# Kernel tuning notes

Hardware: AMD Instinct MI355X
Metric: run time of the kernel (lower is better)

## Reference

```python
import jax, jax.numpy as jnp
import numpy as np
from jax import lax

H_IMG = 224
NUM_HEADS = 8
EPS = 1e-5


def setup_inputs() -> dict:
    key = jax.random.key(0)
    ks = jax.random.split(key, 16)
    C, Dff = 256, 512
    conv_s = 1.0 / np.sqrt(C * 9)
    lin_s = 1.0 / np.sqrt(C)
    lin2_s = 1.0 / np.sqrt(Dff)
    inp = {
        'lidar': jax.random.normal(ks[0], (2, C, H_IMG, H_IMG), jnp.float32),
        'image': jax.random.normal(ks[1], (2, C, H_IMG, H_IMG), jnp.float32),
        'cl_w': jax.random.normal(ks[2], (C, C, 3, 3), jnp.float32) * conv_s,
        'cl_b': jnp.zeros((C,), jnp.float32),
        'bnl_g': jnp.ones((C,), jnp.float32), 'bnl_b': jnp.zeros((C,), jnp.float32),
        'bnl_m': jnp.zeros((C,), jnp.float32), 'bnl_v': jnp.ones((C,), jnp.float32),
        'ci_w': jax.random.normal(ks[3], (C, C, 3, 3), jnp.float32) * conv_s,
        'ci_b': jnp.zeros((C,), jnp.float32),
        'bni_g': jnp.ones((C,), jnp.float32), 'bni_b': jnp.zeros((C,), jnp.float32),
        'bni_m': jnp.zeros((C,), jnp.float32), 'bni_v': jnp.ones((C,), jnp.float32),
        'qw': jax.random.normal(ks[4], (C, C), jnp.float32) * lin_s,
        'qb': jnp.zeros((C,), jnp.float32),
        'kw': jax.random.normal(ks[5], (C, C), jnp.float32) * lin_s,
        'kb': jnp.zeros((C,), jnp.float32),
        'vw': jax.random.normal(ks[6], (C, C), jnp.float32) * lin_s,
        'vb': jnp.zeros((C,), jnp.float32),
        'ow': jax.random.normal(ks[7], (C, C), jnp.float32) * lin_s,
        'ob': jnp.zeros((C,), jnp.float32),
        'ln1_g': jnp.ones((C,), jnp.float32), 'ln1_b': jnp.zeros((C,), jnp.float32),
        'w1': jax.random.normal(ks[8], (C, Dff), jnp.float32) * lin_s,
        'b1': jnp.zeros((Dff,), jnp.float32),
        'w2': jax.random.normal(ks[9], (Dff, C), jnp.float32) * lin2_s,
        'b2': jnp.zeros((C,), jnp.float32),
        'ln2_g': jnp.ones((C,), jnp.float32), 'ln2_b': jnp.zeros((C,), jnp.float32),
        'op_w': jax.random.normal(ks[10], (C, C, 1, 1), jnp.float32) * lin_s,
        'op_b': jnp.zeros((C,), jnp.float32),
        'sp_w': jax.random.normal(ks[11], (C, C, 1, 1), jnp.float32) * lin_s,
        'sp_b': jnp.zeros((C,), jnp.float32),
    }
    return inp


def _conv(x, w, b, stride, pad):
    y = lax.conv_general_dilated(x, w, (stride, stride), ((pad, pad), (pad, pad)),
                                 dimension_numbers=('NCHW', 'OIHW', 'NCHW'))
    return y + b[None, :, None, None]


def _bn(x, g, b, m, v):  # eval-mode BatchNorm2d
    inv = g * lax.rsqrt(v + EPS)
    return x * inv[None, :, None, None] + (b - m * inv)[None, :, None, None]


def _ln(x, g, b):
    mu = jnp.mean(x, -1, keepdims=True)
    var = jnp.mean(jnp.square(x - mu), -1, keepdims=True)
    return (x - mu) * lax.rsqrt(var + EPS) * g + b


def reference(lidar, image, cl_w, cl_b, bnl_g, bnl_b, bnl_m, bnl_v,
              ci_w, ci_b, bni_g, bni_b, bni_m, bni_v,
              qw, qb, kw, kb, vw, vb, ow, ob, ln1_g, ln1_b,
              w1, b1, w2, b2, ln2_g, ln2_b, op_w, op_b, sp_w, sp_b):
    B, C, H, W = lidar.shape
    # spatial compression (stride-4 conv + BN + ReLU)
    lc = jax.nn.relu(_bn(_conv(lidar, cl_w, cl_b, 4, 1), bnl_g, bnl_b, bnl_m, bnl_v))
    ic = jax.nn.relu(_bn(_conv(image, ci_w, ci_b, 4, 1), bni_g, bni_b, bni_m, bni_v))
    _, Ch, Hc, Wc = lc.shape
    N = Hc * Wc
    lseq = lc.reshape(B, Ch, N).transpose(0, 2, 1)  # (B,N,C)
    iseq = ic.reshape(B, Ch, N).transpose(0, 2, 1)

    # cross-attention (lidar queries, image keys/values)
    h, d = NUM_HEADS, Ch // NUM_HEADS
    scale = d ** -0.5
    Q = (lseq @ qw + qb).reshape(B, N, h, d).transpose(0, 2, 1, 3)
    K = (iseq @ kw + kb).reshape(B, N, h, d).transpose(0, 2, 1, 3)
    V = (iseq @ vw + vb).reshape(B, N, h, d).transpose(0, 2, 1, 3)
    scores = jnp.einsum('bhqd,bhkd->bhqk', Q, K) * scale
    attn = jax.nn.softmax(scores, axis=-1)
    ctx = jnp.einsum('bhqk,bhkd->bhqd', attn, V)
    attn_out = ctx.transpose(0, 2, 1, 3).reshape(B, N, Ch) @ ow + ob

    x = _ln(lseq + attn_out, ln1_g, ln1_b)
    ffn = jax.nn.relu(x @ w1 + b1) @ w2 + b2
    x = _ln(x + ffn, ln2_g, ln2_b)

    oc = x.transpose(0, 2, 1).reshape(B, Ch, Hc, Wc)
    up = jax.image.resize(oc, (B, Ch, H, W), method='bilinear')  # align_corners=False semantics
    out = _conv(up, op_w, op_b, 1, 0) + _conv(lidar, sp_w, sp_b, 1, 0)
    return out
```

## Files before the change

kernel.cpp:

```cpp
#include <hip/hip_runtime.h>
#include <hip/hip_bf16.h>

typedef __bf16 bf16;
typedef __attribute__((ext_vector_type(8))) __bf16 bf16x8;
typedef __attribute__((ext_vector_type(4))) __bf16 bf16x4;
typedef __attribute__((ext_vector_type(4))) float f32x4;
typedef __attribute__((ext_vector_type(4))) unsigned int u32x4;

#define LN_EPS 1e-5f

__device__ __forceinline__ void gload16(const void* g, void* l) {
  __builtin_amdgcn_global_load_lds(
      (__attribute__((address_space(1))) void*)g,
      (__attribute__((address_space(3))) void*)l, 16, 0, 0);
}

__device__ __forceinline__ unsigned pk2(float a, float b) {
  unsigned ua = __builtin_bit_cast(unsigned short, (bf16)a);
  unsigned ub = __builtin_bit_cast(unsigned short, (bf16)b);
  return ua | (ub << 16);
}

__device__ __forceinline__ float fexp2(float x) {
  float r;
  asm("v_exp_f32 %0, %1" : "=v"(r) : "v"(x));
  return r;
}


__global__ void bn_prep2_k(const float* cb0, const float* g0, const float* b0,
                           const float* m0, const float* v0, float* sc0, float* sh0,
                           const float* cb1, const float* g1, const float* b1,
                           const float* m1, const float* v1, float* sc1, float* sh1,
                           float* zp) {
  int c = threadIdx.x;
  bool z = blockIdx.x != 0;
  const float* cb = z ? cb1 : cb0;
  const float* g = z ? g1 : g0;
  const float* bb = z ? b1 : b0;
  const float* m = z ? m1 : m0;
  const float* v = z ? v1 : v0;
  float* sc = z ? sc1 : sc0;
  float* sh = z ? sh1 : sh0;
  float s = g[c] * rsqrtf(v[c] + LN_EPS);
  sc[c] = s;
  sh[c] = (cb[c] - m[c]) * s + bb[c];
  if (blockIdx.x == 0) zp[c] = 0.f;
}

__global__ void t_cvt4_k(const float* a0, const float* a1, const float* a2,
                         const float* a3, bf16* o0, bf16* o1, bf16* o2, bf16* o3) {
  __shared__ float tile[32][33];
  int z = blockIdx.z;
  const float* in = z == 0 ? a0 : z == 1 ? a1 : z == 2 ? a2 : a3;
  bf16* out = z == 0 ? o0 : z == 1 ? o1 : z == 2 ? o2 : o3;
  int c0 = blockIdx.x * 32, r0 = blockIdx.y * 32;
  int tx = threadIdx.x, ty = threadIdx.y;
  for (int yy = ty; yy < 32; yy += 8)
    tile[yy][tx] = in[(long)(r0 + yy) * 256 + c0 + tx];
  __syncthreads();
  for (int yy = ty; yy < 32; yy += 8)
    out[(long)(c0 + yy) * 256 + r0 + tx] = (bf16)tile[tx][yy];
}

__global__ void t_cvt_k(const float* __restrict__ in, bf16* __restrict__ out,
                        int R, int Cc) {
  __shared__ float tile[32][33];
  int c0 = blockIdx.x * 32, r0 = blockIdx.y * 32;
  int tx = threadIdx.x, ty = threadIdx.y;
  for (int yy = ty; yy < 32; yy += 8)
    tile[yy][tx] = in[(long)(r0 + yy) * Cc + c0 + tx];
  __syncthreads();
  for (int yy = ty; yy < 32; yy += 8)
    out[(long)(c0 + yy) * R + r0 + tx] = (bf16)tile[tx][yy];
}

__global__ void cvt2_k(const float* a0, const float* a1, bf16* o0, bf16* o1, int n) {
  const float* in = blockIdx.y ? a1 : a0;
  bf16* out = blockIdx.y ? o1 : o0;
  int i = (blockIdx.x * 256 + threadIdx.x) * 4;
  if (i < n) {
    float4 v = *(const float4*)(in + i);
    bf16x4 o = {(bf16)v.x, (bf16)v.y, (bf16)v.z, (bf16)v.w};
    *(bf16x4*)(out + i) = o;
  }
}

__global__ void wprep_k(const float* w0, const float* w1, bf16* o0, bf16* o1) {
  const float* w = blockIdx.y ? w1 : w0;
  bf16* o = blockIdx.y ? o1 : o0;
  int idx = blockIdx.x * 256 + threadIdx.x;
  int co = idx / 2304, r = idx - co * 2304;
  int k9 = r >> 8, ci = r & 255;
  o[idx] = (bf16)w[(co * 256 + ci) * 9 + k9];
}

__global__ __launch_bounds__(256) void t_in_k(const float* __restrict__ lid,
                                              const float* __restrict__ img,
                                              bf16* __restrict__ lidT,
                                              bf16* __restrict__ imgT) {
  int z = blockIdx.z;
  int b = z & 1;
  const float* in = (z < 2) ? lid : img;
  bf16* out = (z < 2) ? lidT : imgT;
  long p0 = (long)blockIdx.x * 128;
  int c0 = blockIdx.y * 128;
  __shared__ unsigned tile[128 * 68];
  int t = threadIdx.x;
  const float* ib = in + (long)b * 256 * 50176;
  bf16* ob = out + (long)b * 50176 * 256;
  int q = t & 31;
  int cp = t >> 5;
#pragma unroll
  for (int pp = 0; pp < 8; ++pp) {
    int chl = pp * 16 + cp * 2;
    const float* s = ib + (long)(c0 + chl) * 50176 + p0 + q * 4;
    float4 a = *(const float4*)s;
    float4 bv = *(const float4*)(s + 50176);
    unsigned wv[4] = {pk2(a.x, bv.x), pk2(a.y, bv.y), pk2(a.z, bv.z),
                      pk2(a.w, bv.w)};
    int c = pp * 8 + cp;
#pragma unroll
    for (int j = 0; j < 4; ++j)
      tile[(q * 4 + j) * 68 + c] = wv[j];
  }
  __syncthreads();
  int c8 = t & 15;
#pragma unroll
  for (int pp = 0; pp < 8; ++pp) {
    int p = pp * 16 + (t >> 4);
    u32x4 vv = *(const u32x4*)&tile[p * 68 + c8 * 4];
    *(u32x4*)(ob + (p0 + p) * 256 + c0 + c8 * 8) = vv;
  }
}

__global__ void t_v_k(const bf16* __restrict__ V, bf16* __restrict__ Vt) {
  __shared__ bf16 tile[32][33];
  int b = blockIdx.z;
  int n0 = blockIdx.x * 32, c0 = blockIdx.y * 32;
  int tx = threadIdx.x, ty = threadIdx.y;
  for (int yy = ty; yy < 32; yy += 8)
    tile[yy][tx] = V[(long)(b * 3136 + n0 + yy) * 256 + c0 + tx];
  __syncthreads();
  for (int yy = ty; yy < 32; yy += 8)
    Vt[(long)(b * 256 + c0 + yy) * 3136 + n0 + tx] = tile[tx][yy];
}

__global__ void ln_k(const float* __restrict__ in, const float* __restrict__ g,
                     const float* __restrict__ bb, float* __restrict__ outf,
                     bf16* __restrict__ outb) {
  int w = threadIdx.x >> 6, l = threadIdx.x & 63;
  long row = (long)blockIdx.x * 4 + w;
  float4 v = *(const float4*)(in + row * 256 + l * 4);
  float s = v.x + v.y + v.z + v.w;
  for (int m = 1; m < 64; m <<= 1) s += __shfl_xor(s, m);
  float mu = s * (1.0f / 256.0f);
  float dx = v.x - mu, dy = v.y - mu, dz = v.z - mu, dw = v.w - mu;
  float q = dx * dx + dy * dy + dz * dz + dw * dw;
  for (int m = 1; m < 64; m <<= 1) q += __shfl_xor(q, m);
  float rstd = rsqrtf(q * (1.0f / 256.0f) + LN_EPS);
  int c = l * 4;
  float y0 = dx * rstd * g[c] + bb[c];
  float y1 = dy * rstd * g[c + 1] + bb[c + 1];
  float y2 = dz * rstd * g[c + 2] + bb[c + 2];
  float y3 = dw * rstd * g[c + 3] + bb[c + 3];
  if (outf) {
    float4 o = {y0, y1, y2, y3};
    *(float4*)(outf + row * 256 + c) = o;
  }
  bf16x4 ob = {(bf16)y0, (bf16)y1, (bf16)y2, (bf16)y3};
  *(bf16x4*)(outb + row * 256 + c) = ob;
}

struct ConvJob {
  const bf16* inT;
  const bf16* wT;
  const float* scale;
  const float* shift;
  bf16* out;
};

__global__ __launch_bounds__(256) void convgemm_k(ConvJob j0, ConvJob j1,
                                                  const bf16* zp) {
  const ConvJob jb = blockIdx.z ? j1 : j0;
  __shared__ bf16 lA[64 * 64];
  __shared__ bf16 lB[64 * 64];
  const int tid = threadIdx.x;
  const int w = tid >> 6, l = tid & 63;
  const int l15 = l & 15;
  const int m0 = blockIdx.x * 64;
  const int n0 = blockIdx.y * 64;
  const int mw = (w >> 1) * 32, nw = (w & 1) * 32;
  f32x4 acc[2][2] = {};
  const int srow = w * 8 + (l >> 3);
  const int kc8 = (l & 7) * 8;
  long rb[2];
  int voy[2], vox[2];
#pragma unroll
  for (int p = 0; p < 2; ++p) {
    int m = m0 + srow + p * 32;
    int b = m / 3136;
    int mm = m - b * 3136;
    int oy = mm / 56, ox = mm - oy * 56;
    rb[p] = ((long)b * 50176 + (long)(4 * oy - 1) * 224 + (4 * ox - 1)) * 256 + kc8;
    voy[p] = oy;
    vox[p] = ox;
  }
  const bf16* Bb = jb.wT + (long)(n0 + srow) * 2304 + kc8;
  bf16* lAp = &lA[srow * 64 + kc8];
  bf16* lBp = &lB[srow * 64 + kc8];
  const bf16* zsrc = zp + kc8;
#pragma unroll
  for (int st = 0; st < 36; ++st) {
    const int k9 = st >> 2, ci0 = (st & 3) * 64;
    const int ky = k9 / 3, kx = k9 - 3 * ky;
    const long koff = (long)(ky * 224 + kx) * 256 + ci0;
#pragma unroll
    for (int p = 0; p < 2; ++p) {
      bool ok = (voy[p] > 0 || ky > 0) && (vox[p] > 0 || kx > 0);
      const bf16* src = ok ? jb.inT + rb[p] + koff : zsrc;
      gload16(src, lAp + p * 32 * 64);
    }
    gload16(Bb + st * 64, lBp);
    gload16(Bb + 32 * 2304 + st * 64, lBp + 32 * 64);
    __syncthreads();
    const int kq = (l >> 4) * 8;
#pragma unroll
    for (int kk = 0; kk < 64; kk += 32) {
      bf16x8 af[2], bfv[2];
#pragma unroll
      for (int i = 0; i < 2; ++i)
        af[i] = *(const bf16x8*)&lA[(mw + i * 16 + l15) * 64 + kk + kq];
#pragma unroll
      for (int j = 0; j < 2; ++j)
        bfv[j] = *(const bf16x8*)&lB[(nw + j * 16 + l15) * 64 + kk + kq];
#pragma unroll
      for (int i = 0; i < 2; ++i)
#pragma unroll
        for (int j = 0; j < 2; ++j)
          acc[i][j] = __builtin_amdgcn_mfma_f32_16x16x32_bf16(af[i], bfv[j],
                                                              acc[i][j], 0, 0, 0);
    }
    __syncthreads();
  }
#pragma unroll
  for (int i = 0; i < 2; ++i)
#pragma unroll
    for (int j = 0; j < 2; ++j)
#pragma unroll
      for (int r = 0; r < 4; ++r) {
        const long row = m0 + mw + i * 16 + (l >> 4) * 4 + r;
        const long col = n0 + nw + j * 16 + l15;
        float v = fmaxf(acc[i][j][r] * jb.scale[col] + jb.shift[col], 0.f);
        jb.out[row * 256 + col] = (bf16)v;
      }
}


struct EpiParams {
  float* out0;
  bf16* out1;
  const float* v0;
  const float* res;
  const bf16* resb;
  int ldc;
  float mul;
};

struct GemmJob {
  const bf16* A;
  const bf16* Bt;
  EpiParams ep;
};

struct GemmJobs3 {
  GemmJob j[3];
};

enum { EPI_QKV = 0, EPI_BIAS_RELU_BF16 = 1, EPI_BIAS_ADD = 2,
       EPI_BIAS_ADDB = 3, EPI_ROWB_F32 = 4, EPI_FINAL2 = 5 };

template <int EPI, int BM, int BN>
__global__ __launch_bounds__(256) void gemm_bt(GemmJobs3 jobs, int K) {
  const GemmJob jb = jobs.j[blockIdx.z];
  const bf16* __restrict__ A = jb.A;
  const bf16* __restrict__ Bt = jb.Bt;
  const EpiParams ep = jb.ep;
  constexpr int MI = (BM == 128 && BN == 128) ? 4 : 2;
  constexpr int NJ = (BN == 128) ? 4 : 2;
  __shared__ bf16 lA[BM * 64];
  __shared__ bf16 lB[BN * 64];
  const int tid = threadIdx.x;
  const int w = tid >> 6, l = tid & 63;
  const int l15 = l & 15;
  const long m0 = (long)blockIdx.x * BM;
  const long n0 = (long)blockIdx.y * BN;
  const int mw = (BM == 128) ? ((BN == 128) ? (w >> 1) * 64 : w * 32)
                             : (w >> 1) * 32;
  const int nw = (BN == 128) ? (w & 1) * 64 : ((BM == 128) ? 0 : (w & 1) * 32);
  f32x4 acc[MI][NJ] = {};
  const int srow = w * 8 + (l >> 3);
  const int kc8 = (l & 7) * 8;
  const bf16* Ab = A + (m0 + srow) * (long)K + kc8;
  const bf16* Bb = Bt + (n0 + srow) * (long)K + kc8;
  bf16* lAp = &lA[srow * 64 + kc8];
  bf16* lBp = &lB[srow * 64 + kc8];
  for (int k0 = 0; k0 < K; k0 += 64) {
#pragma unroll
    for (int p = 0; p < BM / 32; ++p)
      gload16(Ab + (long)p * 32 * K + k0, lAp + p * 32 * 64);
#pragma unroll
    for (int p = 0; p < BN / 32; ++p)
      gload16(Bb + (long)p * 32 * K + k0, lBp + p * 32 * 64);
    __syncthreads();
    const int kq = (l >> 4) * 8;
#pragma unroll
    for (int kk = 0; kk < 64; kk += 32) {
      bf16x8 af[MI], bfv[NJ];
#pragma unroll
      for (int i = 0; i < MI; ++i)
        af[i] = *(const bf16x8*)&lA[(mw + i * 16 + l15) * 64 + kk + kq];
#pragma unroll
      for (int j = 0; j < NJ; ++j)
        bfv[j] = *(const bf16x8*)&lB[(nw + j * 16 + l15) * 64 + kk + kq];
#pragma unroll
      for (int i = 0; i < MI; ++i)
#pragma unroll
        for (int j = 0; j < NJ; ++j)
          acc[i][j] = __builtin_amdgcn_mfma_f32_16x16x32_bf16(af[i], bfv[j],
                                                              acc[i][j], 0, 0, 0);
    }
    __syncthreads();
  }
  const int ldc = ep.ldc;
#pragma unroll
  for (int i = 0; i < MI; ++i)
#pragma unroll
    for (int j = 0; j < NJ; ++j)
#pragma unroll
      for (int r = 0; r < 4; ++r) {
        const long row = m0 + mw + i * 16 + (l >> 4) * 4 + r;
        const long col = n0 + nw + j * 16 + l15;
        float v = acc[i][j][r];
        if constexpr (EPI == EPI_QKV) {
          ep.out1[row * ldc + col] = (bf16)((v + ep.v0[col]) * ep.mul);
        } else if constexpr (EPI == EPI_BIAS_RELU_BF16) {
          ep.out1[row * ldc + col] = (bf16)fmaxf(v + ep.v0[col], 0.f);
        } else if constexpr (EPI == EPI_BIAS_ADD) {
          ep.out0[row * ldc + col] = v + ep.v0[col] + ep.res[row * ldc + col];
        } else if constexpr (EPI == EPI_BIAS_ADDB) {
          ep.out0[row * ldc + col] =
              v + ep.v0[col] + (float)ep.resb[row * ldc + col];
        } else if constexpr (EPI == EPI_ROWB_F32) {
          ep.out0[row * ldc + col] = v + ep.v0[row];
        } else {
          int colp = (int)col;
          int y = colp / 224, x = colp - y * 224;
          int ry = y & 3, rx = x & 3;
          int y0 = (y >> 2) - 1 + (ry >> 1);
          int x0 = (x >> 2) - 1 + (rx >> 1);
          float wy = (ry == 0) ? 0.625f : (ry == 1) ? 0.875f : (ry == 2) ? 0.125f : 0.375f;
          float wx = (rx == 0) ? 0.625f : (rx == 1) ? 0.875f : (rx == 2) ? 0.125f : 0.375f;
          int y0c = y0 > 0 ? y0 : 0, y1c = (y0 + 1) < 55 ? (y0 + 1) : 55;
          int x0c = x0 > 0 ? x0 : 0, x1c = (x0 + 1) < 55 ? (x0 + 1) : 55;
          int co = (int)row;
          const float* ocr = ep.res + (long)co * 3136;
          float v00 = ocr[y0c * 56 + x0c];
          float v01 = ocr[y0c * 56 + x1c];
          float v10 = ocr[y1c * 56 + x0c];
          float v11 = ocr[y1c * 56 + x1c];
          float up = (1.f - wy) * ((1.f - wx) * v00 + wx * v01) +
                     wy * ((1.f - wx) * v10 + wx * v11);
          ep.out0[row * ldc + col] = v + ep.v0[co] + up;
        }
      }
}

__global__ __launch_bounds__(256) void flash_k(const bf16* __restrict__ Qg,
                                               const bf16* __restrict__ Kg,
                                               const bf16* __restrict__ Vt,
                                               bf16* __restrict__ ctx) {
  const int w = threadIdx.x >> 6, l = threadIdx.x & 63;
  const int fid = blockIdx.x;
  const int grp = (fid & 7) * 2 + ((fid >> 3) / 49);
  const int qt = (fid >> 3) % 49;
  const int b = grp >> 3, h = grp & 7;
  const int N = 3136;
  const int l15 = l & 15, g = l >> 4;
  const int q0 = (qt * 4 + w) * 16;
  const int kperm = 8 * (l15 >> 2) + (l15 & 3);
  __shared__ bf16 lds[2][4][512];

  bf16x8 qf = *(const bf16x8*)(Qg + ((long)(b * N + q0 + l15)) * 256 + h * 32 + g * 8);
  const bf16* Kb_ = Kg + ((long)b * N) * 256 + h * 32;
  const bf16* Vb_ = Vt + ((long)(b * 256 + h * 32)) * 3136;
  const long kOffA = (long)kperm * 256 + g * 8;
  const long kOffB = (long)(kperm + 4) * 256 + g * 8;
  const long vOff0 = (long)l15 * 3136 + g * 8;
  const long vOff1 = (long)(16 + l15) * 3136 + g * 8;

  f32x4 o0 = {}, o1 = {};
  float ls = 0.f;

  auto stage = [&](int buf, int kt) {
    const bf16* kp = Kb_ + (long)kt * 32 * 256;
    const bf16* vp = Vb_ + kt * 32;
    if (w == 0)
      gload16(kp + kOffA, &lds[buf][0][l * 8]);
    else if (w == 1)
      gload16(kp + kOffB, &lds[buf][1][l * 8]);
    else if (w == 2)
      gload16(vp + vOff0, &lds[buf][2][l * 8]);
    else
      gload16(vp + vOff1, &lds[buf][3][l * 8]);
  };

  stage(0, 0);
  __syncthreads();
  int cur = 0;
  for (int kt = 0; kt < 98; ++kt) {
    if (kt < 97) stage(cur ^ 1, kt + 1);
    bf16x8 kf0 = *(const bf16x8*)&lds[cur][0][l * 8];
    bf16x8 kf1 = *(const bf16x8*)&lds[cur][1][l * 8];
    bf16x8 vf0 = *(const bf16x8*)&lds[cur][2][l * 8];
    bf16x8 vf1 = *(const bf16x8*)&lds[cur][3][l * 8];
    f32x4 z = {};
    f32x4 s0 = __builtin_amdgcn_mfma_f32_16x16x32_bf16(kf0, qf, z, 0, 0, 0);
    f32x4 s1 = __builtin_amdgcn_mfma_f32_16x16x32_bf16(kf1, qf, z, 0, 0, 0);
    float p0 = fexp2(s0[0]), p1 = fexp2(s0[1]), p2 = fexp2(s0[2]), p3 = fexp2(s0[3]);
    float p4 = fexp2(s1[0]), p5 = fexp2(s1[1]), p6 = fexp2(s1[2]), p7 = fexp2(s1[3]);
    ls += ((p0 + p1) + (p2 + p3)) + ((p4 + p5) + (p6 + p7));
    u32x4 fp;
    fp[0] = pk2(p0, p1);
    fp[1] = pk2(p2, p3);
    fp[2] = pk2(p4, p5);
    fp[3] = pk2(p6, p7);
    bf16x8 pf = __builtin_bit_cast(bf16x8, fp);
    o0 = __builtin_amdgcn_mfma_f32_16x16x32_bf16(vf0, pf, o0, 0, 0, 0);
    o1 = __builtin_amdgcn_mfma_f32_16x16x32_bf16(vf1, pf, o1, 0, 0, 0);
    __syncthreads();
    cur ^= 1;
  }
  ls += __shfl_xor(ls, 16);
  ls += __shfl_xor(ls, 32);
  float inv = 1.0f / ls;
  long base = ((long)(b * N + q0 + l15)) * 256 + h * 32;
  bf16x4 ov0 = {(bf16)(o0[0] * inv), (bf16)(o0[1] * inv),
                (bf16)(o0[2] * inv), (bf16)(o0[3] * inv)};
  bf16x4 ov1 = {(bf16)(o1[0] * inv), (bf16)(o1[1] * inv),
                (bf16)(o1[2] * inv), (bf16)(o1[3] * inv)};
  *(bf16x4*)(ctx + base + g * 4) = ov0;
  *(bf16x4*)(ctx + base + 16 + g * 4) = ov1;
}


extern "C" void kernel_launch(void* const* d_in, const int* in_sizes, int n_in,
                              void* d_out, int out_size, void* d_ws, size_t ws_size,
                              hipStream_t stream) {
  const float* lidar = (const float*)d_in[0];
  const float* image = (const float*)d_in[1];
  const float* cl_w = (const float*)d_in[2];
  const float* cl_b = (const float*)d_in[3];
  const float* bnl_g = (const float*)d_in[4];
  const float* bnl_b = (const float*)d_in[5];
  const float* bnl_m = (const float*)d_in[6];
  const float* bnl_v = (const float*)d_in[7];
  const float* ci_w = (const float*)d_in[8];
  const float* ci_b = (const float*)d_in[9];
  const float* bni_g = (const float*)d_in[10];
  const float* bni_b = (const float*)d_in[11];
  const float* bni_m = (const float*)d_in[12];
  const float* bni_v = (const float*)d_in[13];
  const float* qw = (const float*)d_in[14];
  const float* qb = (const float*)d_in[15];
  const float* kw = (const float*)d_in[16];
  const float* kb = (const float*)d_in[17];
  const float* vw = (const float*)d_in[18];
  const float* vb = (const float*)d_in[19];
  const float* ow = (const float*)d_in[20];
  const float* ob = (const float*)d_in[21];
  const float* ln1_g = (const float*)d_in[22];
  const float* ln1_b = (const float*)d_in[23];
  const float* w1 = (const float*)d_in[24];
  const float* b1 = (const float*)d_in[25];
  const float* w2 = (const float*)d_in[26];
  const float* b2 = (const float*)d_in[27];
  const float* ln2_g = (const float*)d_in[28];
  const float* ln2_b = (const float*)d_in[29];
  const float* op_w = (const float*)d_in[30];
  const float* op_b = (const float*)d_in[31];
  const float* sp_w = (const float*)d_in[32];
  const float* sp_b = (const float*)d_in[33];
  float* out = (float*)d_out;

  char* ws = (char*)d_ws;
  bf16* lidT = (bf16*)ws;
  bf16* imgT = (bf16*)(ws + 51380224);
  char* ov = ws + 51380224;
  bf16* Qb = (bf16*)(ov + 0);
  bf16* Kb = (bf16*)(ov + 3211264);
  bf16* Vb = (bf16*)(ov + 6422528);
  bf16* Vt = (bf16*)(ov + 9633792);
  bf16* ctx = (bf16*)(ov + 12845056);
  bf16* x_b = (bf16*)(ov + 16056320);
  float* tmp1 = (float*)(ov + 19267584);
  float* x_f = (float*)(ov + 25690112);
  bf16* hmid = (bf16*)(ov + 32112640);
  float* oc2T = (float*)(ov + 38535168);
  size_t off = 102760448;
  auto carve = [&](size_t bytes) {
    void* p = ws + off;
    off += (bytes + 255) & ~(size_t)255;
    return p;
  };
  bf16* lseq_b = (bf16*)carve(3211264);
  bf16* iseq_b = (bf16*)carve(3211264);
  bf16* qwT = (bf16*)carve(131072);
  bf16* kwT = (bf16*)carve(131072);
  bf16* vwT = (bf16*)carve(131072);
  bf16* owT = (bf16*)carve(131072);
  bf16* w1t = (bf16*)carve(262144);
  bf16* w2t = (bf16*)carve(262144);
  bf16* clwT = (bf16*)carve(1179648);
  bf16* ciwT = (bf16*)carve(1179648);
  bf16* opwB = (bf16*)carve(131072);
  bf16* spwB = (bf16*)carve(131072);
  float* scale_l = (float*)carve(1024);
  float* shift_l = (float*)carve(1024);
  float* scale_i = (float*)carve(1024);
  float* shift_i = (float*)carve(1024);
  float* zp = (float*)carve(1024);
  float* tmp2 = tmp1;
  bf16* x2_pad = (bf16*)(void*)x_f;

  dim3 b32x8(32, 8);
  const float qscale = 0.17677669529663687f * 1.4426950408889634f;

  bn_prep2_k<<<2, 256, 0, stream>>>(cl_b, bnl_g, bnl_b, bnl_m, bnl_v, scale_l, shift_l,
                                    ci_b, bni_g, bni_b, bni_m, bni_v, scale_i, shift_i,
                                    zp);
  t_cvt4_k<<<dim3(8, 8, 4), b32x8, 0, stream>>>(qw, kw, vw, ow, qwT, kwT, vwT, owT);
  t_cvt_k<<<dim3(16, 8), b32x8, 0, stream>>>(w1, w1t, 256, 512);
  t_cvt_k<<<dim3(8, 16), b32x8, 0, stream>>>(w2, w2t, 512, 256);
  cvt2_k<<<dim3(64, 2), 256, 0, stream>>>(op_w, sp_w, opwB, spwB, 65536);
  wprep_k<<<dim3(2304, 2), 256, 0, stream>>>(cl_w, ci_w, clwT, ciwT);

  t_in_k<<<dim3(392, 2, 4), 256, 0, stream>>>(lidar, image, lidT, imgT);

  {
    ConvJob j0{lidT, clwT, scale_l, shift_l, lseq_b};
    ConvJob j1{imgT, ciwT, scale_i, shift_i, iseq_b};
    convgemm_k<<<dim3(98, 4, 2), 256, 0, stream>>>(j0, j1, (const bf16*)zp);
  }
  {
    GemmJobs3 js{};
    js.j[0] = {lseq_b, qwT, {nullptr, Qb, qb, nullptr, nullptr, 256, qscale}};
    js.j[1] = {iseq_b, kwT, {nullptr, Kb, kb, nullptr, nullptr, 256, 1.f}};
    js.j[2] = {iseq_b, vwT, {nullptr, Vb, vb, nullptr, nullptr, 256, 1.f}};
    gemm_bt<EPI_QKV, 64, 64><<<dim3(98, 4, 3), 256, 0, stream>>>(js, 256);
  }
  t_v_k<<<dim3(98, 8, 2), b32x8, 0, stream>>>(Vb, Vt);
  flash_k<<<dim3(784), 256, 0, stream>>>(Qb, Kb, Vt, ctx);
  {
    GemmJobs3 js{};
    js.j[0] = {ctx, owT, {tmp1, nullptr, ob, nullptr, lseq_b, 256, 1.f}};
    gemm_bt<EPI_BIAS_ADDB, 64, 64><<<dim3(98, 4, 1), 256, 0, stream>>>(js, 256);
  }
  ln_k<<<1568, 256, 0, stream>>>(tmp1, ln1_g, ln1_b, x_f, x_b);
  {
    GemmJobs3 js{};
    js.j[0] = {x_b, w1t, {nullptr, hmid, b1, nullptr, nullptr, 512, 1.f}};
    gemm_bt<EPI_BIAS_RELU_BF16, 64, 64><<<dim3(98, 8, 1), 256, 0, stream>>>(js, 256);
  }
  {
    GemmJobs3 js{};
    js.j[0] = {hmid, w2t, {tmp2, nullptr, b2, x_f, nullptr, 256, 1.f}};
    gemm_bt<EPI_BIAS_ADD, 64, 64><<<dim3(98, 4, 1), 256, 0, stream>>>(js, 512);
  }
  ln_k<<<1568, 256, 0, stream>>>(tmp2, ln2_g, ln2_b, nullptr, x2_pad);
  {
    GemmJobs3 js{};
    js.j[0] = {opwB, x2_pad, {oc2T, nullptr, op_b, nullptr, nullptr, 3136, 1.f}};
    js.j[1] = {opwB, x2_pad + (long)3136 * 256,
               {oc2T + (long)256 * 3136, nullptr, op_b, nullptr, nullptr, 3136, 1.f}};
    gemm_bt<EPI_ROWB_F32, 64, 64><<<dim3(4, 49, 2), 256, 0, stream>>>(js, 256);
  }
  {
    GemmJobs3 js{};
    js.j[0] = {spwB, lidT, {out, nullptr, sp_b, oc2T, nullptr, 50176, 1.f}};
    js.j[1] = {spwB, lidT + (long)50176 * 256,
               {out + (long)256 * 50176, nullptr, sp_b,
                oc2T + (long)256 * 3136, nullptr, 50176, 1.f}};
    gemm_bt<EPI_FINAL2, 64, 64><<<dim3(4, 784, 2), 256, 0, stream>>>(js, 256);
  }
}
```

Measured before the change: 323.5 us.

## Use channel-blocked packed layout for transposed inputs, drop LDS transpose

The input conversion kernel now writes lidar/image as bf16 in a [b][channel-group of 8][pixel][8] layout, so each thread reads 8 strided channel values and writes one 16-byte vector, with no shared-memory tile. The conv-GEMM and the final 1x1 GEMM (new BPACK template path) compute their addresses from this packed layout. The aim is to make the transpose pass cheaper, in exchange for more scattered 16-byte gathers in the downstream GEMM loads, which can hurt their coalescing.

```diff
diff --git a/kernel.cpp b/kernel.cpp
--- a/kernel.cpp
+++ b/kernel.cpp
@@ -99,39 +99,18 @@
                                               const float* __restrict__ img,
                                               bf16* __restrict__ lidT,
                                               bf16* __restrict__ imgT) {
+  int t = threadIdx.x;
+  int p = blockIdx.x * 256 + t;
+  int cg = blockIdx.y;
   int z = blockIdx.z;
   int b = z & 1;
   const float* in = (z < 2) ? lid : img;
   bf16* out = (z < 2) ? lidT : imgT;
-  long p0 = (long)blockIdx.x * 128;
-  int c0 = blockIdx.y * 128;
-  __shared__ unsigned tile[128 * 68];
-  int t = threadIdx.x;
-  const float* ib = in + (long)b * 256 * 50176;
-  bf16* ob = out + (long)b * 50176 * 256;
-  int q = t & 31;
-  int cp = t >> 5;
-#pragma unroll
-  for (int pp = 0; pp < 8; ++pp) {
-    int chl = pp * 16 + cp * 2;
-    const float* s = ib + (long)(c0 + chl) * 50176 + p0 + q * 4;
-    float4 a = *(const float4*)s;
-    float4 bv = *(const float4*)(s + 50176);
-    unsigned wv[4] = {pk2(a.x, bv.x), pk2(a.y, bv.y), pk2(a.z, bv.z),
-                      pk2(a.w, bv.w)};
-    int c = pp * 8 + cp;
-#pragma unroll
-    for (int j = 0; j < 4; ++j)
-      tile[(q * 4 + j) * 68 + c] = wv[j];
-  }
-  __syncthreads();
-  int c8 = t & 15;
-#pragma unroll
-  for (int pp = 0; pp < 8; ++pp) {
-    int p = pp * 16 + (t >> 4);
-    u32x4 vv = *(const u32x4*)&tile[p * 68 + c8 * 4];
-    *(u32x4*)(ob + (p0 + p) * 256 + c0 + c8 * 8) = vv;
-  }
+  const float* src = in + ((long)b * 256 + cg * 8) * 50176 + p;
+  bf16x8 v;
+#pragma unroll
+  for (int j = 0; j < 8; ++j) v[j] = (bf16)src[(long)j * 50176];
+  *(bf16x8*)(out + (((long)b * 32 + cg) * 50176 + p) * 8) = v;
 }
 
 __global__ void t_v_k(const bf16* __restrict__ V, bf16* __restrict__ Vt) {
@@ -202,23 +181,24 @@
     int b = m / 3136;
     int mm = m - b * 3136;
     int oy = mm / 56, ox = mm - oy * 56;
-    rb[p] = ((long)b * 50176 + (long)(4 * oy - 1) * 224 + (4 * ox - 1)) * 256 + kc8;
+    rb[p] = (long)b * 32 * 50176 * 8 + (long)((4 * oy - 1) * 224 + (4 * ox - 1)) * 8;
     voy[p] = oy;
     vox[p] = ox;
   }
+  const long ol = (long)(l & 7) * 50176 * 8;
   const bf16* Bb = jb.wT + (long)(n0 + srow) * 2304 + kc8;
   bf16* lAp = &lA[srow * 64 + kc8];
   bf16* lBp = &lB[srow * 64 + kc8];
   const bf16* zsrc = zp + kc8;
 #pragma unroll
   for (int st = 0; st < 36; ++st) {
-    const int k9 = st >> 2, ci0 = (st & 3) * 64;
+    const int k9 = st >> 2;
     const int ky = k9 / 3, kx = k9 - 3 * ky;
-    const long koff = (long)(ky * 224 + kx) * 256 + ci0;
+    const long koff = (long)(st & 3) * 8 * 50176 * 8 + (long)(ky * 224 + kx) * 8;
 #pragma unroll
     for (int p = 0; p < 2; ++p) {
       bool ok = (voy[p] > 0 || ky > 0) && (vox[p] > 0 || kx > 0);
-      const bf16* src = ok ? jb.inT + rb[p] + koff : zsrc;
+      const bf16* src = ok ? jb.inT + rb[p] + ol + koff : zsrc;
       gload16(src, lAp + p * 32 * 64);
     }
     gload16(Bb + st * 64, lBp);
@@ -280,7 +260,7 @@
 enum { EPI_QKV = 0, EPI_BIAS_RELU_BF16 = 1, EPI_BIAS_ADD = 2,
        EPI_BIAS_ADDB = 3, EPI_ROWB_F32 = 4, EPI_FINAL2 = 5 };
 
-template <int EPI, int BM, int BN>
+template <int EPI, int BM, int BN, int BPACK = 0>
 __global__ __launch_bounds__(256) void gemm_bt(GemmJobs3 jobs, int K) {
   const GemmJob jb = jobs.j[blockIdx.z];
   const bf16* __restrict__ A = jb.A;
@@ -310,8 +290,15 @@
     for (int p = 0; p < BM / 32; ++p)
       gload16(Ab + (long)p * 32 * K + k0, lAp + p * 32 * 64);
 #pragma unroll
-    for (int p = 0; p < BN / 32; ++p)
-      gload16(Bb + (long)p * 32 * K + k0, lBp + p * 32 * 64);
+    for (int p = 0; p < BN / 32; ++p) {
+      if constexpr (BPACK) {
+        const bf16* src = Bt + ((long)(k0 >> 3) + (l & 7)) * 50176 * 8 +
+                          (n0 + srow + p * 32) * 8;
+        gload16(src, lBp + p * 32 * 64);
+      } else {
+        gload16(Bb + (long)p * 32 * K + k0, lBp + p * 32 * 64);
+      }
+    }
     __syncthreads();
     const int kq = (l >> 4) * 8;
 #pragma unroll
@@ -545,7 +532,7 @@
   cvt2_k<<<dim3(64, 2), 256, 0, stream>>>(op_w, sp_w, opwB, spwB, 65536);
   wprep_k<<<dim3(2304, 2), 256, 0, stream>>>(cl_w, ci_w, clwT, ciwT);
 
-  t_in_k<<<dim3(392, 2, 4), 256, 0, stream>>>(lidar, image, lidT, imgT);
+  t_in_k<<<dim3(196, 32, 4), 256, 0, stream>>>(lidar, image, lidT, imgT);
 
   {
     ConvJob j0{lidT, clwT, scale_l, shift_l, lseq_b};
@@ -588,9 +575,9 @@
   {
     GemmJobs3 js{};
     js.j[0] = {spwB, lidT, {out, nullptr, sp_b, oc2T, nullptr, 50176, 1.f}};
-    js.j[1] = {spwB, lidT + (long)50176 * 256,
+    js.j[1] = {spwB, lidT + (long)12845056,
                {out + (long)256 * 50176, nullptr, sp_b,
                 oc2T + (long)256 * 3136, nullptr, 50176, 1.f}};
-    gemm_bt<EPI_FINAL2, 64, 64><<<dim3(4, 784, 2), 256, 0, stream>>>(js, 256);
-  }
-}
+    gemm_bt<EPI_FINAL2, 64, 64, 1><<<dim3(4, 784, 2), 256, 0, stream>>>(js, 256);
+  }
+}
```

After: 411.9 us. 1.27x slower.
